# Optimization experiments

Hardware: AMD Instinct MI355X
Metric: run time of the kernel (lower is better)

The kernel has to match this reference:

```python
import jax, jax.numpy as jnp
import numpy as np

D_MODEL = 1024


def setup_inputs() -> dict:
    key = jax.random.key(0)
    k_x, k_qkv, k_proj, k_b = jax.random.split(key, 4)
    b, t, d = 4, 2048, D_MODEL
    scale = 1.0 / np.sqrt(d)
    x = jax.random.normal(k_x, (b, t, d), dtype=jnp.float32)
    # torch Linear(d, 3d, bias=False): weight [3d, d]; we store transposed [d, 3d]
    w_qkv = jax.random.normal(k_qkv, (d, 3 * d), dtype=jnp.float32) * scale
    w_proj = jax.random.normal(k_proj, (d, d), dtype=jnp.float32) * scale
    b_proj = jax.random.normal(k_b, (d,), dtype=jnp.float32) * scale
    return {"x": x, "w_qkv": w_qkv, "w_proj": w_proj, "b_proj": b_proj}


def reference(x, w_qkv, w_proj, b_proj):
    b, t, d = x.shape
    qkv = jnp.einsum("btd,de->bte", x, w_qkv)  # [b, t, 3d]
    q, k, v = jnp.split(qkv, 3, axis=-1)
    att = jnp.einsum("btd,bsd->bts", q, k) / jnp.sqrt(jnp.float32(d))  # [b, t, t]
    causal = jnp.tril(jnp.ones((t, t), dtype=bool))
    att = jnp.where(causal, att, -jnp.inf)
    att = jax.nn.softmax(att, axis=-1)
    out = jnp.einsum("bts,bsd->btd", att, v)
    return jnp.einsum("btd,de->bte", out, w_proj) + b_proj
```

## Files before the change

### kernel.cpp

```cpp
#include <hip/hip_runtime.h>


typedef __bf16 bf16x8_t __attribute__((ext_vector_type(8)));
typedef float  f32x16_t __attribute__((ext_vector_type(16)));
typedef unsigned short u16;

struct alignas(8) u16x4 { u16 x, y, z, w; };

__device__ inline float bf2f(u16 u) {
  union { unsigned u; float f; } c; c.u = ((unsigned)u) << 16; return c.f;
}
__device__ inline u16 f2bf(float f) {
  union { float f; unsigned u; } c; c.f = f;
  unsigned r = c.u + 0x7fffu + ((c.u >> 16) & 1u);
  return (u16)(r >> 16);
}

template<int OUTMODE, int GRIDMODE>
__global__ __launch_bounds__(256, 4)
void gemm_bt(const u16* __restrict__ A, const u16* __restrict__ B,
             void* __restrict__ Cv, u16* __restrict__ C2,
             const float* __restrict__ bias,
             int K, int lda, int ldb, int ldc,
             long sA, long sB, long sC)
{
  int bn0, bm0;
  if (GRIDMODE == 1) {
    const int x = blockIdx.x;
    int r = (int)((sqrtf(8.f * x + 1.f) - 1.f) * 0.5f);
    while ((r + 1) * (r + 2) / 2 <= x) ++r;
    while (r * (r + 1) / 2 > x) --r;
    bm0 = r * 128;
    bn0 = (x - r * (r + 1) / 2) * 128;
  } else if (GRIDMODE == 2) {
    bn0 = blockIdx.x * 128;
    bm0 = ((int)gridDim.y - 1 - (int)blockIdx.y) * 128;
  } else {
    bn0 = blockIdx.x * 128;
    bm0 = blockIdx.y * 128;
  }
  const long bz = blockIdx.z;
  const u16* Ab = A + bz * sA;
  const u16* Bb = B + bz * sB;
  const int Keff = (GRIDMODE == 2) ? min(K, bm0 + 128) : K;

  __shared__ __align__(16) u16 lA[128 * 64];
  __shared__ __align__(16) u16 lB[128 * 64];

  const int tid  = threadIdx.x;
  const int lane = tid & 63;
  const int wv   = tid >> 6;
  const int wm   = (wv >> 1) << 6;
  const int wn   = (wv & 1) << 6;
  const int ml   = lane & 31;
  const int kh   = lane >> 5;
  const int swz  = ml & 7;

  f32x16_t acc[2][2];
#pragma unroll
  for (int i = 0; i < 2; ++i)
#pragma unroll
    for (int j = 0; j < 2; ++j)
#pragma unroll
      for (int r = 0; r < 16; ++r)
        acc[i][j][r] = 0.f;

  float rsacc = 0.f;

  const long ldA2 = (long)lda * 2, ldB2 = (long)ldb * 2;
  const int rowA = tid >> 3;
  const int csw  = (tid & 7) ^ (rowA & 7);
  const char* pA = (const char*)(Ab + (long)bm0 * lda) + (long)rowA * ldA2 + (csw << 4);
  const char* pB = (const char*)(Bb + (long)bn0 * ldb) + (long)rowA * ldB2 + (csw << 4);
  const int ldsbo = tid * 16;

  for (int k0 = 0; k0 < Keff; k0 += 64) {
    const long kb = (long)k0 * 2;
#pragma unroll
    for (int r = 0; r < 4; ++r)
      __builtin_amdgcn_global_load_lds(
          (const __attribute__((address_space(1))) unsigned int*)(pA + kb + (long)(r * 32) * ldA2),
          (__attribute__((address_space(3))) unsigned int*)((char*)lA + ldsbo + r * 4096), 16, 0, 0);
#pragma unroll
    for (int r = 0; r < 4; ++r)
      __builtin_amdgcn_global_load_lds(
          (const __attribute__((address_space(1))) unsigned int*)(pB + kb + (long)(r * 32) * ldB2),
          (__attribute__((address_space(3))) unsigned int*)((char*)lB + ldsbo + r * 4096), 16, 0, 0);
    __syncthreads();

#pragma unroll
    for (int s = 0; s < 4; ++s) {
      const int ck = ((s * 2 + kh) ^ swz) << 3;
      bf16x8_t a0 = *(const bf16x8_t*)&lA[(wm + ml) * 64 + ck];
      bf16x8_t a1 = *(const bf16x8_t*)&lA[(wm + 32 + ml) * 64 + ck];
      bf16x8_t b0 = *(const bf16x8_t*)&lB[(wn + ml) * 64 + ck];
      bf16x8_t b1 = *(const bf16x8_t*)&lB[(wn + 32 + ml) * 64 + ck];
      acc[0][0] = __builtin_amdgcn_mfma_f32_32x32x16_bf16(a0, b0, acc[0][0], 0, 0, 0);
      acc[0][1] = __builtin_amdgcn_mfma_f32_32x32x16_bf16(a0, b1, acc[0][1], 0, 0, 0);
      acc[1][0] = __builtin_amdgcn_mfma_f32_32x32x16_bf16(a1, b0, acc[1][0], 0, 0, 0);
      acc[1][1] = __builtin_amdgcn_mfma_f32_32x32x16_bf16(a1, b1, acc[1][1], 0, 0, 0);
    }

    if (OUTMODE == 4) {
      const int rr = tid >> 1;
      const int hh = (tid & 1) << 2;
#pragma unroll
      for (int c = 0; c < 4; ++c) {
        const int cc = hh + ((c + rr) & 3);
        bf16x8_t v = *(const bf16x8_t*)&lA[rr * 64 + cc * 8];
#pragma unroll
        for (int e = 0; e < 8; ++e) rsacc += (float)v[e];
      }
    }
    __syncthreads();
  }

  if (OUTMODE == 2) {
    if (bn0 >= 2048) {
#pragma unroll
      for (int i = 0; i < 2; ++i) {
#pragma unroll
        for (int g = 0; g < 4; ++g) {
          const int rowb = bm0 + wm + i * 32 + g * 8 + kh * 4;
          const int b_  = rowb >> 11;
          const int s_  = rowb & 2047;
#pragma unroll
          for (int j = 0; j < 2; ++j) {
            const int dcol = bn0 - 2048 + wn + j * 32 + ml;
            u16x4 o = {f2bf(acc[i][j][g * 4 + 0]), f2bf(acc[i][j][g * 4 + 1]),
                       f2bf(acc[i][j][g * 4 + 2]), f2bf(acc[i][j][g * 4 + 3])};
            *(u16x4*)&C2[(((long)b_ * 1024 + dcol) << 11) + s_] = o;
          }
        }
      }
    } else {
      u16* Cb16 = (u16*)Cv;
#pragma unroll
      for (int i = 0; i < 2; ++i)
#pragma unroll
        for (int j = 0; j < 2; ++j)
#pragma unroll
          for (int reg = 0; reg < 16; ++reg) {
            const int row = bm0 + wm + i * 32 + (reg & 3) + 8 * (reg >> 2) + kh * 4;
            const int col = bn0 + wn + j * 32 + ml;
            Cb16[(long)row * ldc + col] = f2bf(acc[i][j][reg]);
          }
    }
    return;
  }

  if (OUTMODE == 3) {
    const float scale = 0.03125f;
    const bool diag = (bm0 == bn0);
    u16* Cb16 = (u16*)Cv + bz * sC;
#pragma unroll
    for (int i = 0; i < 2; ++i) {
#pragma unroll
      for (int reg = 0; reg < 16; ++reg) {
        const int grow = bm0 + wm + i * 32 + (reg & 3) + 8 * (reg >> 2) + kh * 4;
        const int col0 = bn0 + wn + ml;
        float e0 = (diag && col0 > grow)      ? 0.f : __expf(acc[i][0][reg] * scale);
        float e1 = (diag && col0 + 32 > grow) ? 0.f : __expf(acc[i][1][reg] * scale);
        Cb16[(long)grow * ldc + col0]      = f2bf(e0);
        Cb16[(long)grow * ldc + col0 + 32] = f2bf(e1);
      }
    }
    return;
  }

  if (OUTMODE == 4) {
    float* rsl = (float*)lA;
    rsl[tid] = rsacc;
    __syncthreads();
    float* rinv = (float*)lB;
    if (tid < 128) rinv[tid] = 1.0f / (rsl[2 * tid] + rsl[2 * tid + 1]);
    __syncthreads();
    u16* Cb16 = (u16*)Cv + bz * sC;
#pragma unroll
    for (int i = 0; i < 2; ++i)
#pragma unroll
      for (int j = 0; j < 2; ++j)
#pragma unroll
        for (int reg = 0; reg < 16; ++reg) {
          const int rl  = wm + i * 32 + (reg & 3) + 8 * (reg >> 2) + kh * 4;
          const int col = bn0 + wn + j * 32 + ml;
          Cb16[(long)(bm0 + rl) * ldc + col] = f2bf(acc[i][j][reg] * rinv[rl]);
        }
    return;
  }

  float* Cf32 = (float*)Cv + bz * sC;
#pragma unroll
  for (int i = 0; i < 2; ++i)
#pragma unroll
    for (int j = 0; j < 2; ++j)
#pragma unroll
      for (int reg = 0; reg < 16; ++reg) {
        const int row = bm0 + wm + i * 32 + (reg & 3) + 8 * (reg >> 2) + kh * 4;
        const int col = bn0 + wn + j * 32 + ml;
        Cf32[(long)row * ldc + col] = acc[i][j][reg] + bias[col];
      }
}

__global__ __launch_bounds__(256)
void cvt_f32_bf16(const float* __restrict__ in, u16* __restrict__ out) {
  const int i = blockIdx.x * 256 + threadIdx.x;
  float4 v = ((const float4*)in)[i];
  u16x4 o = {f2bf(v.x), f2bf(v.y), f2bf(v.z), f2bf(v.w)};
  ((u16x4*)out)[i] = o;
}

__global__ __launch_bounds__(256)
void transpose_weights(const float* __restrict__ wqkv, u16* __restrict__ wqkvT,
                       const float* __restrict__ wproj, u16* __restrict__ wprojT) {
  const bool isq = blockIdx.x < 96;
  const float* in = isq ? wqkv : wproj;
  u16* out        = isq ? wqkvT : wprojT;
  const int C     = isq ? 3072 : 1024;
  const int c0 = (isq ? blockIdx.x : (blockIdx.x - 96)) * 32;
  const int r0 = blockIdx.y * 32;
  __shared__ float t[32][33];
  const int tx = threadIdx.x & 31, ty = threadIdx.x >> 5;
#pragma unroll
  for (int i = 0; i < 32; i += 8)
    t[ty + i][tx] = in[(long)(r0 + ty + i) * C + (c0 + tx)];
  __syncthreads();
#pragma unroll
  for (int i = 0; i < 32; i += 8)
    out[(long)(c0 + ty + i) * 1024 + (r0 + tx)] = f2bf(t[tx][ty + i]);
}

extern "C" void kernel_launch(void* const* d_in, const int* in_sizes, int n_in,
                              void* d_out, int out_size, void* d_ws, size_t ws_size,
                              hipStream_t stream) {
  (void)in_sizes; (void)n_in; (void)out_size; (void)ws_size;
  const float* x      = (const float*)d_in[0];
  const float* w_qkv  = (const float*)d_in[1];
  const float* w_proj = (const float*)d_in[2];
  const float* b_proj = (const float*)d_in[3];
  float* y = (float*)d_out;
  char*  ws = (char*)d_ws;

  u16* xbf    = (u16*)(ws);
  u16* qk     = (u16*)(ws + (16l << 20));
  u16* wqkvT  = (u16*)(ws + (48l << 20));
  u16* wprojT = (u16*)(ws + (54l << 20));
  u16* vT     = (u16*)(ws + (56l << 20));
  u16* E      = (u16*)(ws + (72l << 20));
  u16* attn   = xbf;

  cvt_f32_bf16<<<8192, 256, 0, stream>>>(x, xbf);
  transpose_weights<<<dim3(128, 32), 256, 0, stream>>>(w_qkv, wqkvT, w_proj, wprojT);
  gemm_bt<2, 0><<<dim3(24, 64, 1), 256, 0, stream>>>(
      xbf, wqkvT, qk, vT, nullptr, 1024, 1024, 1024, 2048, 0, 0, 0);
  gemm_bt<3, 1><<<dim3(136, 1, 4), 256, 0, stream>>>(
      qk, qk + 1024, E, nullptr, nullptr, 1024, 2048, 2048, 2048,
      (long)2048 * 2048, (long)2048 * 2048, (long)2048 * 2048);
  gemm_bt<4, 2><<<dim3(8, 16, 4), 256, 0, stream>>>(
      E, vT, attn, nullptr, nullptr, 2048, 2048, 2048, 1024,
      (long)2048 * 2048, (long)1024 * 2048, (long)2048 * 1024);
  gemm_bt<1, 0><<<dim3(8, 64, 1), 256, 0, stream>>>(
      attn, wprojT, y, nullptr, b_proj, 1024, 1024, 1024, 1024, 0, 0, 0);
}
```

Baseline: 274.3 us.

## Switch GEMM to 16x16x32 MFMA with split-K LDS layout and fuse prep kernels

Replaces the 32x32x16 bf16 MFMA tiling with 16x16x32 MFMAs, using a 4x4 grid of fragments per wave. LDS is re-laid out as two 32-wide K halves with a new XOR swizzle, and every epilogue is remapped to the new accumulator layout. The input conversion and weight transpose kernels are also merged into one launch to save a kernel launch. The new layout and swizzle risk bank conflicts or extra LDS reads if the mapping is off.

```diff
diff --git a/kernel.cpp b/kernel.cpp
--- a/kernel.cpp
+++ b/kernel.cpp
@@ -2,7 +2,7 @@
 
 
 typedef __bf16 bf16x8_t __attribute__((ext_vector_type(8)));
-typedef float  f32x16_t __attribute__((ext_vector_type(16)));
+typedef float  f32x4_t  __attribute__((ext_vector_type(4)));
 typedef unsigned short u16;
 
 struct alignas(8) u16x4 { u16 x, y, z, w; };
@@ -44,107 +44,111 @@
   const u16* Bb = B + bz * sB;
   const int Keff = (GRIDMODE == 2) ? min(K, bm0 + 128) : K;
 
-  __shared__ __align__(16) u16 lA[128 * 64];
-  __shared__ __align__(16) u16 lB[128 * 64];
+  __shared__ __align__(16) u16 lA[2 * 128 * 32];
+  __shared__ __align__(16) u16 lB[2 * 128 * 32];
 
   const int tid  = threadIdx.x;
   const int lane = tid & 63;
   const int wv   = tid >> 6;
   const int wm   = (wv >> 1) << 6;
   const int wn   = (wv & 1) << 6;
-  const int ml   = lane & 31;
-  const int kh   = lane >> 5;
-  const int swz  = ml & 7;
-
-  f32x16_t acc[2][2];
-#pragma unroll
-  for (int i = 0; i < 2; ++i)
-#pragma unroll
-    for (int j = 0; j < 2; ++j)
-#pragma unroll
-      for (int r = 0; r < 16; ++r)
-        acc[i][j][r] = 0.f;
+  const int l15  = lane & 15;
+  const int rd_off = l15 * 64 + ((((lane >> 4) ^ (l15 >> 1)) & 3) << 4);
+
+  f32x4_t acc[4][4];
+#pragma unroll
+  for (int i = 0; i < 4; ++i)
+#pragma unroll
+    for (int j = 0; j < 4; ++j)
+      acc[i][j] = (f32x4_t){0.f, 0.f, 0.f, 0.f};
 
   float rsacc = 0.f;
 
   const long ldA2 = (long)lda * 2, ldB2 = (long)ldb * 2;
-  const int rowA = tid >> 3;
-  const int csw  = (tid & 7) ^ (rowA & 7);
-  const char* pA = (const char*)(Ab + (long)bm0 * lda) + (long)rowA * ldA2 + (csw << 4);
-  const char* pB = (const char*)(Bb + (long)bn0 * ldb) + (long)rowA * ldB2 + (csw << 4);
+  const int c_src = (tid & 3) ^ ((tid >> 3) & 3);
+  const char* pA = (const char*)(Ab + (long)bm0 * lda) + (long)(tid >> 2) * ldA2 + (c_src << 4);
+  const char* pB = (const char*)(Bb + (long)bn0 * ldb) + (long)(tid >> 2) * ldB2 + (c_src << 4);
   const int ldsbo = tid * 16;
 
   for (int k0 = 0; k0 < Keff; k0 += 64) {
     const long kb = (long)k0 * 2;
 #pragma unroll
-    for (int r = 0; r < 4; ++r)
+    for (int r = 0; r < 4; ++r) {
+      const long go = (long)(r & 1) * 64 * ldA2 + (r >> 1) * 64;
       __builtin_amdgcn_global_load_lds(
-          (const __attribute__((address_space(1))) unsigned int*)(pA + kb + (long)(r * 32) * ldA2),
+          (const __attribute__((address_space(1))) unsigned int*)(pA + kb + go),
           (__attribute__((address_space(3))) unsigned int*)((char*)lA + ldsbo + r * 4096), 16, 0, 0);
-#pragma unroll
-    for (int r = 0; r < 4; ++r)
+    }
+#pragma unroll
+    for (int r = 0; r < 4; ++r) {
+      const long go = (long)(r & 1) * 64 * ldB2 + (r >> 1) * 64;
       __builtin_amdgcn_global_load_lds(
-          (const __attribute__((address_space(1))) unsigned int*)(pB + kb + (long)(r * 32) * ldB2),
+          (const __attribute__((address_space(1))) unsigned int*)(pB + kb + go),
           (__attribute__((address_space(3))) unsigned int*)((char*)lB + ldsbo + r * 4096), 16, 0, 0);
-    __syncthreads();
-
-#pragma unroll
-    for (int s = 0; s < 4; ++s) {
-      const int ck = ((s * 2 + kh) ^ swz) << 3;
-      bf16x8_t a0 = *(const bf16x8_t*)&lA[(wm + ml) * 64 + ck];
-      bf16x8_t a1 = *(const bf16x8_t*)&lA[(wm + 32 + ml) * 64 + ck];
-      bf16x8_t b0 = *(const bf16x8_t*)&lB[(wn + ml) * 64 + ck];
-      bf16x8_t b1 = *(const bf16x8_t*)&lB[(wn + 32 + ml) * 64 + ck];
-      acc[0][0] = __builtin_amdgcn_mfma_f32_32x32x16_bf16(a0, b0, acc[0][0], 0, 0, 0);
-      acc[0][1] = __builtin_amdgcn_mfma_f32_32x32x16_bf16(a0, b1, acc[0][1], 0, 0, 0);
-      acc[1][0] = __builtin_amdgcn_mfma_f32_32x32x16_bf16(a1, b0, acc[1][0], 0, 0, 0);
-      acc[1][1] = __builtin_amdgcn_mfma_f32_32x32x16_bf16(a1, b1, acc[1][1], 0, 0, 0);
+    }
+    __syncthreads();
+
+    const char* lAb = (const char*)lA + wm * 64 + rd_off;
+    const char* lBb = (const char*)lB + wn * 64 + rd_off;
+#pragma unroll
+    for (int s = 0; s < 2; ++s) {
+      const int so = s * 8192;
+      bf16x8_t b0 = *(const bf16x8_t*)(lBb + so + 0 * 1024);
+      bf16x8_t b1 = *(const bf16x8_t*)(lBb + so + 1 * 1024);
+      bf16x8_t b2 = *(const bf16x8_t*)(lBb + so + 2 * 1024);
+      bf16x8_t b3 = *(const bf16x8_t*)(lBb + so + 3 * 1024);
+#pragma unroll
+      for (int mf = 0; mf < 4; ++mf) {
+        bf16x8_t a = *(const bf16x8_t*)(lAb + so + mf * 1024);
+        acc[mf][0] = __builtin_amdgcn_mfma_f32_16x16x32_bf16(a, b0, acc[mf][0], 0, 0, 0);
+        acc[mf][1] = __builtin_amdgcn_mfma_f32_16x16x32_bf16(a, b1, acc[mf][1], 0, 0, 0);
+        acc[mf][2] = __builtin_amdgcn_mfma_f32_16x16x32_bf16(a, b2, acc[mf][2], 0, 0, 0);
+        acc[mf][3] = __builtin_amdgcn_mfma_f32_16x16x32_bf16(a, b3, acc[mf][3], 0, 0, 0);
+      }
     }
 
     if (OUTMODE == 4) {
       const int rr = tid >> 1;
-      const int hh = (tid & 1) << 2;
+      const int bsel = (tid & 1) * 8192;
 #pragma unroll
       for (int c = 0; c < 4; ++c) {
-        const int cc = hh + ((c + rr) & 3);
-        bf16x8_t v = *(const bf16x8_t*)&lA[rr * 64 + cc * 8];
+        const int cc = (c + (rr >> 1)) & 3;
+        bf16x8_t v = *(const bf16x8_t*)((const char*)lA + bsel + rr * 64 + cc * 16);
 #pragma unroll
         for (int e = 0; e < 8; ++e) rsacc += (float)v[e];
       }
     }
     __syncthreads();
   }
+
+  const int r4 = (lane >> 4) << 2;
 
   if (OUTMODE == 2) {
     if (bn0 >= 2048) {
 #pragma unroll
-      for (int i = 0; i < 2; ++i) {
-#pragma unroll
-        for (int g = 0; g < 4; ++g) {
-          const int rowb = bm0 + wm + i * 32 + g * 8 + kh * 4;
-          const int b_  = rowb >> 11;
-          const int s_  = rowb & 2047;
-#pragma unroll
-          for (int j = 0; j < 2; ++j) {
-            const int dcol = bn0 - 2048 + wn + j * 32 + ml;
-            u16x4 o = {f2bf(acc[i][j][g * 4 + 0]), f2bf(acc[i][j][g * 4 + 1]),
-                       f2bf(acc[i][j][g * 4 + 2]), f2bf(acc[i][j][g * 4 + 3])};
-            *(u16x4*)&C2[(((long)b_ * 1024 + dcol) << 11) + s_] = o;
-          }
+      for (int mf = 0; mf < 4; ++mf) {
+        const int s0 = bm0 + wm + mf * 16 + r4;
+        const int b_ = s0 >> 11;
+        const int s_ = s0 & 2047;
+#pragma unroll
+        for (int nf = 0; nf < 4; ++nf) {
+          const int dcol = bn0 - 2048 + wn + nf * 16 + l15;
+          u16x4 o = {f2bf(acc[mf][nf][0]), f2bf(acc[mf][nf][1]),
+                     f2bf(acc[mf][nf][2]), f2bf(acc[mf][nf][3])};
+          *(u16x4*)&C2[(((long)b_ * 1024 + dcol) << 11) + s_] = o;
         }
       }
     } else {
       u16* Cb16 = (u16*)Cv;
 #pragma unroll
-      for (int i = 0; i < 2; ++i)
-#pragma unroll
-        for (int j = 0; j < 2; ++j)
-#pragma unroll
-          for (int reg = 0; reg < 16; ++reg) {
-            const int row = bm0 + wm + i * 32 + (reg & 3) + 8 * (reg >> 2) + kh * 4;
-            const int col = bn0 + wn + j * 32 + ml;
-            Cb16[(long)row * ldc + col] = f2bf(acc[i][j][reg]);
-          }
+      for (int mf = 0; mf < 4; ++mf)
+#pragma unroll
+        for (int nf = 0; nf < 4; ++nf) {
+          const int col = bn0 + wn + nf * 16 + l15;
+#pragma unroll
+          for (int r = 0; r < 4; ++r)
+            Cb16[(long)(bm0 + wm + mf * 16 + r4 + r) * ldc + col] = f2bf(acc[mf][nf][r]);
+        }
     }
     return;
   }
@@ -154,17 +158,17 @@
     const bool diag = (bm0 == bn0);
     u16* Cb16 = (u16*)Cv + bz * sC;
 #pragma unroll
-    for (int i = 0; i < 2; ++i) {
-#pragma unroll
-      for (int reg = 0; reg < 16; ++reg) {
-        const int grow = bm0 + wm + i * 32 + (reg & 3) + 8 * (reg >> 2) + kh * 4;
-        const int col0 = bn0 + wn + ml;
-        float e0 = (diag && col0 > grow)      ? 0.f : __expf(acc[i][0][reg] * scale);
-        float e1 = (diag && col0 + 32 > grow) ? 0.f : __expf(acc[i][1][reg] * scale);
-        Cb16[(long)grow * ldc + col0]      = f2bf(e0);
-        Cb16[(long)grow * ldc + col0 + 32] = f2bf(e1);
-      }
-    }
+    for (int mf = 0; mf < 4; ++mf)
+#pragma unroll
+      for (int r = 0; r < 4; ++r) {
+        const int grow = bm0 + wm + mf * 16 + r4 + r;
+#pragma unroll
+        for (int nf = 0; nf < 4; ++nf) {
+          const int col = bn0 + wn + nf * 16 + l15;
+          float e = (diag && col > grow) ? 0.f : __expf(acc[mf][nf][r] * scale);
+          Cb16[(long)grow * ldc + col] = f2bf(e);
+        }
+      }
     return;
   }
 
@@ -177,48 +181,53 @@
     __syncthreads();
     u16* Cb16 = (u16*)Cv + bz * sC;
 #pragma unroll
-    for (int i = 0; i < 2; ++i)
-#pragma unroll
-      for (int j = 0; j < 2; ++j)
-#pragma unroll
-        for (int reg = 0; reg < 16; ++reg) {
-          const int rl  = wm + i * 32 + (reg & 3) + 8 * (reg >> 2) + kh * 4;
-          const int col = bn0 + wn + j * 32 + ml;
-          Cb16[(long)(bm0 + rl) * ldc + col] = f2bf(acc[i][j][reg] * rinv[rl]);
-        }
+    for (int mf = 0; mf < 4; ++mf)
+#pragma unroll
+      for (int nf = 0; nf < 4; ++nf) {
+        const int col = bn0 + wn + nf * 16 + l15;
+#pragma unroll
+        for (int r = 0; r < 4; ++r) {
+          const int rl = wm + mf * 16 + r4 + r;
+          Cb16[(long)(bm0 + rl) * ldc + col] = f2bf(acc[mf][nf][r] * rinv[rl]);
+        }
+      }
     return;
   }
 
   float* Cf32 = (float*)Cv + bz * sC;
 #pragma unroll
-  for (int i = 0; i < 2; ++i)
-#pragma unroll
-    for (int j = 0; j < 2; ++j)
-#pragma unroll
-      for (int reg = 0; reg < 16; ++reg) {
-        const int row = bm0 + wm + i * 32 + (reg & 3) + 8 * (reg >> 2) + kh * 4;
-        const int col = bn0 + wn + j * 32 + ml;
-        Cf32[(long)row * ldc + col] = acc[i][j][reg] + bias[col];
-      }
+  for (int mf = 0; mf < 4; ++mf)
+#pragma unroll
+    for (int nf = 0; nf < 4; ++nf) {
+      const int col = bn0 + wn + nf * 16 + l15;
+      const float bb = bias[col];
+#pragma unroll
+      for (int r = 0; r < 4; ++r)
+        Cf32[(long)(bm0 + wm + mf * 16 + r4 + r) * ldc + col] = acc[mf][nf][r] + bb;
+    }
 }
 
 __global__ __launch_bounds__(256)
-void cvt_f32_bf16(const float* __restrict__ in, u16* __restrict__ out) {
-  const int i = blockIdx.x * 256 + threadIdx.x;
-  float4 v = ((const float4*)in)[i];
-  u16x4 o = {f2bf(v.x), f2bf(v.y), f2bf(v.z), f2bf(v.w)};
-  ((u16x4*)out)[i] = o;
-}
-
-__global__ __launch_bounds__(256)
-void transpose_weights(const float* __restrict__ wqkv, u16* __restrict__ wqkvT,
-                       const float* __restrict__ wproj, u16* __restrict__ wprojT) {
-  const bool isq = blockIdx.x < 96;
+void prep(const float* __restrict__ x, u16* __restrict__ xbf,
+          const float* __restrict__ wqkv, u16* __restrict__ wqkvT,
+          const float* __restrict__ wproj, u16* __restrict__ wprojT) {
+  const int bid = blockIdx.x;
+  if (bid < 8192) {
+    const int i = bid * 256 + threadIdx.x;
+    float4 v = ((const float4*)x)[i];
+    u16x4 o = {f2bf(v.x), f2bf(v.y), f2bf(v.z), f2bf(v.w)};
+    ((u16x4*)xbf)[i] = o;
+    return;
+  }
+  const int tb = bid - 8192;
+  const int bx = tb & 127;
+  const int by = tb >> 7;
+  const bool isq = bx < 96;
   const float* in = isq ? wqkv : wproj;
   u16* out        = isq ? wqkvT : wprojT;
   const int C     = isq ? 3072 : 1024;
-  const int c0 = (isq ? blockIdx.x : (blockIdx.x - 96)) * 32;
-  const int r0 = blockIdx.y * 32;
+  const int c0 = (isq ? bx : (bx - 96)) * 32;
+  const int r0 = by * 32;
   __shared__ float t[32][33];
   const int tx = threadIdx.x & 31, ty = threadIdx.x >> 5;
 #pragma unroll
@@ -249,8 +258,7 @@
   u16* E      = (u16*)(ws + (72l << 20));
   u16* attn   = xbf;
 
-  cvt_f32_bf16<<<8192, 256, 0, stream>>>(x, xbf);
-  transpose_weights<<<dim3(128, 32), 256, 0, stream>>>(w_qkv, wqkvT, w_proj, wprojT);
+  prep<<<12288, 256, 0, stream>>>(x, xbf, w_qkv, wqkvT, w_proj, wprojT);
   gemm_bt<2, 0><<<dim3(24, 64, 1), 256, 0, stream>>>(
       xbf, wqkvT, qk, vT, nullptr, 1024, 1024, 1024, 2048, 0, 0, 0);
   gemm_bt<3, 1><<<dim3(136, 1, 4), 256, 0, stream>>>(
```

Measured after the change: 261.3 us. 4.7% less time.
